# Kernel tuning notes

Hardware: AMD Instinct MI355X
Metric: run time of the kernel (lower is better)

The kernel has to match this reference:

```python
import jax, jax.numpy as jnp
import numpy as np

B, S, D, H = 4, 8192, 1024, 16
DH = D // H  # attention head size


def setup_inputs() -> dict:
    key = jax.random.key(0)
    ks = jax.random.split(key, 12)
    sc = 0.02
    return {
        "hidden_states": jax.random.normal(ks[0], (B, S, D), jnp.float32),
        "attention_mask": jnp.zeros((B, 1, S), jnp.float32),
        "Wq": jax.random.normal(ks[1], (D, D), jnp.float32) * sc,
        "bq": jnp.zeros((D,), jnp.float32),
        "Wqa": jax.random.normal(ks[2], (D, H), jnp.float32) * sc,
        "bqa": jnp.zeros((H,), jnp.float32),
        "Wk": jax.random.normal(ks[3], (D, D), jnp.float32) * sc,
        "bk": jnp.zeros((D,), jnp.float32),
        "Wka": jax.random.normal(ks[4], (D, H), jnp.float32) * sc,
        "bka": jnp.zeros((H,), jnp.float32),
        "Wt": jax.random.normal(ks[5], (D, D), jnp.float32) * sc,
        "bt": jnp.zeros((D,), jnp.float32),
    }


def reference(hidden_states, attention_mask, Wq, bq, Wqa, bqa, Wk, bk, Wka, bka, Wt, bt):
    b, s, _ = hidden_states.shape
    scale = 1.0 / np.sqrt(DH).astype(np.float32)

    mixed_q = hidden_states @ Wq + bq            # [B,S,D]
    mixed_k = hidden_states @ Wk + bk            # [B,S,D]

    # query attention pooling: scores [B,H,S]
    q_score = (mixed_q @ Wqa + bqa).transpose(0, 2, 1) * scale + attention_mask
    q_weight = jax.nn.softmax(q_score, axis=-1)  # [B,H,S]

    q_heads = mixed_q.reshape(b, s, H, DH)       # [B,S,H,DH]
    pooled_q = jnp.einsum("bhs,bshd->bhd", q_weight, q_heads)  # [B,H,DH]
    pooled_q = pooled_q.reshape(b, 1, D)         # global query vector per batch

    mixed_qk = mixed_k * pooled_q                # [B,S,D]

    qk_score = (mixed_qk @ Wka + bka).transpose(0, 2, 1) * scale + attention_mask
    qk_weight = jax.nn.softmax(qk_score, axis=-1)  # [B,H,S]

    k_heads = mixed_qk.reshape(b, s, H, DH)
    pooled_k = jnp.einsum("bhs,bshd->bhd", qk_weight, k_heads)  # [B,H,DH]

    weighted = (q_heads * pooled_k[:, None, :, :]).reshape(b, s, D)  # [B,S,D]
    return weighted @ Wt + bt + mixed_q
```

## Files before the change

### kernel.cpp

```cpp
#include <hip/hip_runtime.h>
#include <hip/hip_bf16.h>
#include <stdint.h>

typedef __hip_bfloat16 bf16;
typedef __attribute__((ext_vector_type(8))) short bf16x8v;
typedef __attribute__((ext_vector_type(4))) float f32x4v;

#define B_   4
#define S_   8192
#define D_   1024
#define H_   16
#define DH_  64
#define M_TOT (B_ * S_)

__device__ __forceinline__ float bf2f(bf16 x) { return __bfloat162float(x); }
__device__ __forceinline__ bf16  f2bf(float x) { return __float2bfloat16(x); }

__device__ __forceinline__ void storev(float* p, float v) { *p = v; }
__device__ __forceinline__ void storev(bf16* p, float v) { *p = f2bf(v); }

__device__ __forceinline__ void async_copy16(const void* g, void* l) {
  __builtin_amdgcn_global_load_lds(
      (const __attribute__((address_space(1))) unsigned int*)g,
      (__attribute__((address_space(3))) unsigned int*)l,
      16, 0, 0);
}

#define VMCNT(n) asm volatile("s_waitcnt vmcnt(" #n ")" ::: "memory")
__device__ __forceinline__ void barrier_() {
  asm volatile("" ::: "memory");
  __builtin_amdgcn_s_barrier();
  asm volatile("" ::: "memory");
}

__global__ __launch_bounds__(256) void f2bf_kernel(
    const float* __restrict__ in, bf16* __restrict__ out, int n4)
{
  const int i = blockIdx.x * 256 + threadIdx.x;
  if (i >= n4) return;
  const float4 v = ((const float4*)in)[i];
  union { bf16 h[4]; uint64_t u; } pk;
  pk.h[0] = f2bf(v.x); pk.h[1] = f2bf(v.y);
  pk.h[2] = f2bf(v.z); pk.h[3] = f2bf(v.w);
  ((uint64_t*)out)[i] = pk.u;
}

#define STAGE_A(nb, h, k0) do { \
  async_copy16(gA + (size_t)((h) * 64      ) * sA + (size_t)(k0) * 2, smem + (nb) + (h) * 16384 + ldsw); \
  async_copy16(gA + (size_t)((h) * 64 + 128) * sA + (size_t)(k0) * 2, smem + (nb) + (h) * 16384 + 8192 + ldsw); \
} while (0)

#define STAGE_B(nb, h, k0) do { \
  async_copy16(gB + (size_t)((h) * 32      ) * sB + (size_t)(k0) * 2, smem + (nb) + 32768 + (h) * 16384 + ldsw); \
  async_copy16(gB + (size_t)((h) * 32 + 128) * sB + (size_t)(k0) * 2, smem + (nb) + 32768 + (h) * 16384 + 8192 + ldsw); \
} while (0)

#define READ_A(mh) do { \
  _Pragma("unroll") for (int il = 0; il < 4; ++il) { \
    const uint8_t* p_ = Ab + (mh) * 16384 + (wr * 64 + il * 16 + l16) * 128; \
    a[il][0] = *(const bf16x8v*)(p_ + k0off); \
    a[il][1] = *(const bf16x8v*)(p_ + k1off); } \
} while (0)

#define READ_B(nh, BR) do { \
  _Pragma("unroll") for (int jl = 0; jl < 2; ++jl) { \
    const uint8_t* p_ = Bb + 32768 + (nh) * 16384 + (wc * 32 + jl * 16 + l16) * 128; \
    BR[jl][0] = *(const bf16x8v*)(p_ + k0off); \
    BR[jl][1] = *(const bf16x8v*)(p_ + k1off); } \
} while (0)

#define MFMA_Q(IOFF, JOFF, BR) do { \
  _Pragma("unroll") for (int il = 0; il < 4; ++il) \
  _Pragma("unroll") for (int jl = 0; jl < 2; ++jl) \
  _Pragma("unroll") for (int kk = 0; kk < 2; ++kk) \
    acc[(IOFF) + il][(JOFF) + jl] = __builtin_amdgcn_mfma_f32_16x16x32_bf16( \
        a[il][kk], BR[jl][kk], acc[(IOFF) + il][(JOFF) + jl], 0, 0, 0); \
} while (0)

template <typename OutT>
__global__ __launch_bounds__(512, 2) void gemm256_kernel(
    const bf16* __restrict__ A, int lda, const bf16* __restrict__ BT,
    const float* __restrict__ bias0, const float* __restrict__ bias1,
    const bf16* addC, int ldadd,
    OutT* __restrict__ C, int ldc, int M, int Ncols, int K, int perBatchB)
{
  extern __shared__ __align__(16) uint8_t smem[];

  const int ntile = Ncols >> 8;
  const int mtiles = M >> 8;
  const int xcd = blockIdx.x & 7;
  const int local = blockIdx.x >> 3;
  const int tn = local % ntile;
  const int tm = xcd * (mtiles >> 3) + local / ntile;
  const int m0 = tm << 8, n0 = tn << 8;
  const bf16* Bt = BT + (perBatchB ? (size_t)(m0 >> 13) * (size_t)Ncols * (size_t)K : 0);

  const int tid = threadIdx.x, w = tid >> 6, lane = tid & 63;
  const int quad = lane >> 4, l16 = lane & 15;
  const int wr = w >> 2, wc = w & 3;
  const int lr = lane >> 3, ls = lane & 7;

  const size_t sA = (size_t)lda * 2, sB = (size_t)K * 2;
  const int srcslot = (ls ^ lr) << 4;
  const uint8_t* gA = (const uint8_t*)A  + (size_t)(m0 + 8 * w + lr) * sA + srcslot;
  const uint8_t* gB = (const uint8_t*)Bt + (size_t)(n0 + 64 * wr + 8 * wc + lr) * sB + srcslot;
  const int ldsw = w << 10;

  const int e7 = l16 & 7;
  const int k0off = (quad ^ e7) << 4;
  const int k1off = ((quad + 4) ^ e7) << 4;

  f32x4v acc[8][4] = {};
  bf16x8v a[4][2], b0[2][2], b1[2][2];

  const int NT = K >> 6;

  STAGE_A(0, 0, 0);
  STAGE_B(0, 0, 0);
  STAGE_B(0, 1, 0);
  STAGE_A(0, 1, 0);
  VMCNT(4);
  barrier_();

  for (int t = 0; t < NT; ++t) {
    const int buf = (t & 1) << 16;
    const int nbuf = buf ^ 65536;
    const int kst = (t + 1 < NT ? t + 1 : t) << 6;
    const uint8_t* Ab = smem + buf;
    const uint8_t* Bb = smem + buf;

    READ_A(0);
    READ_B(0, b0);
    STAGE_A(nbuf, 0, kst);
    barrier_();
    __builtin_amdgcn_s_setprio(1);
    MFMA_Q(0, 0, b0);
    __builtin_amdgcn_s_setprio(0);
    VMCNT(4);
    barrier_();

    READ_B(1, b1);
    STAGE_B(nbuf, 0, kst);
    barrier_();
    __builtin_amdgcn_s_setprio(1);
    MFMA_Q(0, 2, b1);
    __builtin_amdgcn_s_setprio(0);
    VMCNT(4);
    barrier_();

    READ_A(1);
    STAGE_B(nbuf, 1, kst);
    barrier_();
    __builtin_amdgcn_s_setprio(1);
    MFMA_Q(4, 2, b1);
    __builtin_amdgcn_s_setprio(0);
    barrier_();

    STAGE_A(nbuf, 1, kst);
    barrier_();
    __builtin_amdgcn_s_setprio(1);
    MFMA_Q(4, 0, b0);
    __builtin_amdgcn_s_setprio(0);
    VMCNT(4);
    barrier_();
  }
  VMCNT(0);

#pragma unroll
  for (int ai = 0; ai < 8; ++ai) {
    const int row = m0 + wr * 128 + ai * 16 + quad * 4;
#pragma unroll
    for (int jb = 0; jb < 4; ++jb) {
      const int col = n0 + wc * 64 + jb * 16 + l16;
      const float bb = (col < 1024) ? (bias0 ? bias0[col] : 0.f)
                                    : (bias1 ? bias1[col - 1024] : 0.f);
      f32x4v v = acc[ai][jb];
#pragma unroll
      for (int r = 0; r < 4; ++r) {
        float o = v[r] + bb;
        if (addC) o += bf2f(addC[(size_t)(row + r) * ldadd + col]);
        storev(&C[(size_t)(row + r) * ldc + col], o);
      }
    }
  }
}

__global__ __launch_bounds__(256) void score_kernel(
    const bf16* __restrict__ X, int ldx, const bf16* __restrict__ WaT,
    float* __restrict__ scores, int perBatchW)
{
  const int tid = threadIdx.x, wave = tid >> 6, lane = tid & 63;
  const int quad = lane >> 4, l16 = lane & 15;
  const int row0 = blockIdx.x * 64 + wave * 16;
  const int b = row0 / S_;
  const bf16* W = WaT + (perBatchW ? (size_t)b * H_ * D_ : 0);
  const bf16* arow = X + (size_t)(row0 + l16) * ldx;
  const bf16* brow = W + (size_t)l16 * D_;
  f32x4v acc = {};
  for (int k0 = 0; k0 < D_; k0 += 32) {
    bf16x8v av = *(const bf16x8v*)(arow + k0 + quad * 8);
    bf16x8v bv = *(const bf16x8v*)(brow + k0 + quad * 8);
    acc = __builtin_amdgcn_mfma_f32_16x16x32_bf16(av, bv, acc, 0, 0, 0);
  }
  const int srel = (row0 % S_) + quad * 4;
  float* orow = scores + ((size_t)b * H_ + l16) * S_ + srel;
#pragma unroll
  for (int r = 0; r < 4; r++) orow[r] = acc[r];
}

__global__ __launch_bounds__(256) void stats_kernel(
    const float* __restrict__ sc, const float* __restrict__ mask,
    float scale, float* __restrict__ stats)
{
  const int bh = blockIdx.x, b = bh >> 4, tid = threadIdx.x;
  const float* row = sc + (size_t)bh * S_;
  const float* mrow = mask + (size_t)b * S_;
  __shared__ float red[256];
  float m = -3.4e38f;
  for (int s = tid; s < S_; s += 256) m = fmaxf(m, row[s] * scale + mrow[s]);
  red[tid] = m; __syncthreads();
  for (int o = 128; o > 0; o >>= 1) { if (tid < o) red[tid] = fmaxf(red[tid], red[tid + o]); __syncthreads(); }
  const float M = red[0]; __syncthreads();
  float sum = 0.f;
  for (int s = tid; s < S_; s += 256) sum += expf(row[s] * scale + mrow[s] - M);
  red[tid] = sum; __syncthreads();
  for (int o = 128; o > 0; o >>= 1) { if (tid < o) red[tid] += red[tid + o]; __syncthreads(); }
  if (tid == 0) { stats[bh * 2] = M; stats[bh * 2 + 1] = red[0]; }
}

__global__ __launch_bounds__(256) void pool_kernel(
    const float* __restrict__ sc, const float* __restrict__ mask,
    const float* __restrict__ stats, const bf16* __restrict__ X, int ldx,
    float* __restrict__ pooled, float scale)
{
  const int bh = blockIdx.x, chunk = blockIdx.y;
  const int b = bh >> 4, h = bh & 15;
  const int dh = threadIdx.x & 63, sr = threadIdx.x >> 6;
  const float M = stats[bh * 2], inv = 1.f / stats[bh * 2 + 1];
  const float* row = sc + (size_t)bh * S_;
  const float* mrow = mask + (size_t)b * S_;
  float acc = 0.f;
  const int s0 = chunk * 256;
  for (int s = s0 + sr; s < s0 + 256; s += 4) {
    float w = expf(row[s] * scale + mrow[s] - M) * inv;
    acc += w * bf2f(X[((size_t)b * S_ + s) * ldx + h * DH_ + dh]);
  }
  __shared__ float red[256];
  red[threadIdx.x] = acc; __syncthreads();
  if (sr == 0)
    atomicAdd(&pooled[b * D_ + h * DH_ + dh],
              red[dh] + red[64 + dh] + red[128 + dh] + red[192 + dh]);
}

__global__ __launch_bounds__(256) void prep_wa_kernel(
    const float* __restrict__ Wa, const float* __restrict__ pq,
    bf16* __restrict__ out, int nb)
{
  const int idx = blockIdx.x * 256 + threadIdx.x;
  if (idx >= nb * H_ * D_) return;
  const int d = idx & (D_ - 1);
  const int h = (idx >> 10) & 15;
  const int b = idx >> 14;
  float v = Wa[d * H_ + h];
  if (pq) v *= pq[b * D_ + d];
  out[idx] = f2bf(v);
}

__global__ __launch_bounds__(1024) void transpose_kernel(
    const float* __restrict__ W, bf16* __restrict__ WT)
{
  __shared__ float t[32][33];
  const int tx = threadIdx.x, ty = threadIdx.y;
  const int bx = blockIdx.x, by = blockIdx.y;
  t[ty][tx] = W[(size_t)(by * 32 + ty) * D_ + bx * 32 + tx];
  __syncthreads();
  WT[(size_t)(bx * 32 + ty) * D_ + by * 32 + tx] = f2bf(t[tx][ty]);
}

__global__ __launch_bounds__(1024) void transpose_scale_kernel(
    const float* __restrict__ W, const float* __restrict__ pq,
    const float* __restrict__ pk, bf16* __restrict__ out)
{
  __shared__ float t[32][33];
  const int tx = threadIdx.x, ty = threadIdx.y;
  const int bx = blockIdx.x, by = blockIdx.y, b = blockIdx.z;
  t[ty][tx] = W[(size_t)(by * 32 + ty) * D_ + bx * 32 + tx];
  __syncthreads();
  const int n = bx * 32 + ty, k = by * 32 + tx;
  const float s = pq[b * D_ + k] * pk[b * D_ + k];
  out[(size_t)b * D_ * D_ + (size_t)n * D_ + k] = f2bf(t[tx][ty] * s);
}

namespace {
struct LdsAttrInit {
  LdsAttrInit() {
    (void)hipFuncSetAttribute(reinterpret_cast<const void*>(&gemm256_kernel<bf16>),
                              hipFuncAttributeMaxDynamicSharedMemorySize, 131072);
    (void)hipFuncSetAttribute(reinterpret_cast<const void*>(&gemm256_kernel<float>),
                              hipFuncAttributeMaxDynamicSharedMemorySize, 131072);
  }
};
LdsAttrInit ldsAttrInit_;
}

extern "C" void kernel_launch(void* const* d_in, const int* in_sizes, int n_in,
                              void* d_out, int out_size, void* d_ws, size_t ws_size,
                              hipStream_t stream)
{
  const float* hs   = (const float*)d_in[0];
  const float* mask = (const float*)d_in[1];
  const float* Wq   = (const float*)d_in[2];
  const float* bq   = (const float*)d_in[3];
  const float* Wqa  = (const float*)d_in[4];
  const float* Wk   = (const float*)d_in[6];
  const float* bk   = (const float*)d_in[7];
  const float* Wka  = (const float*)d_in[8];
  const float* Wt   = (const float*)d_in[10];
  const float* bt   = (const float*)d_in[11];
  float* out = (float*)d_out;

  uint8_t* w = (uint8_t*)d_ws;
  bf16*  hs_bf     = (bf16*)(w + 0);
  bf16*  mixed_qk  = (bf16*)(w + 67108864);
  bf16*  WqkT      = (bf16*)(w + 201326592);
  bf16*  WtTs      = (bf16*)(w + 205520896);
  bf16*  WaqT      = (bf16*)(w + 213909504);
  bf16*  WakTs     = (bf16*)(w + 213942272);
  float* scores_q  = (float*)(w + 214073344);
  float* scores_qk = (float*)(w + 216170496);
  float* stats_q   = (float*)(w + 218267648);
  float* stats_qk  = (float*)(w + 218268160);
  float* pq_raw    = (float*)(w + 218268672);
  float* pk_raw    = (float*)(w + 218285056);

  const bf16* mixed_q = mixed_qk;
  const bf16* mixed_k = mixed_qk + 1024;
  const int LDQK = 2048;

  const float scale = 0.125f;
  dim3 tblk(32, 32);

  f2bf_kernel<<<(M_TOT * D_ / 4 + 255) / 256, 256, 0, stream>>>(hs, hs_bf, M_TOT * D_ / 4);

  transpose_kernel<<<dim3(32, 32), tblk, 0, stream>>>(Wq, WqkT);
  transpose_kernel<<<dim3(32, 32), tblk, 0, stream>>>(Wk, WqkT + 1024 * 1024);

  gemm256_kernel<bf16><<<1024, 512, 131072, stream>>>(
      hs_bf, 1024, WqkT, bq, bk, nullptr, 0, mixed_qk, LDQK, M_TOT, 2048, D_, 0);

  hipMemsetAsync(pq_raw, 0, 2 * D_ * B_ * sizeof(float), stream);

  prep_wa_kernel<<<64, 256, 0, stream>>>(Wqa, nullptr, WaqT, 1);
  score_kernel<<<512, 256, 0, stream>>>(mixed_q, LDQK, WaqT, scores_q, 0);
  stats_kernel<<<64, 256, 0, stream>>>(scores_q, mask, scale, stats_q);
  pool_kernel<<<dim3(64, 32), 256, 0, stream>>>(scores_q, mask, stats_q, mixed_q, LDQK, pq_raw, scale);

  prep_wa_kernel<<<256, 256, 0, stream>>>(Wka, pq_raw, WakTs, 4);
  score_kernel<<<512, 256, 0, stream>>>(mixed_k, LDQK, WakTs, scores_qk, 1);
  stats_kernel<<<64, 256, 0, stream>>>(scores_qk, mask, scale, stats_qk);
  pool_kernel<<<dim3(64, 32), 256, 0, stream>>>(scores_qk, mask, stats_qk, mixed_k, LDQK, pk_raw, scale);

  transpose_scale_kernel<<<dim3(32, 32, 4), tblk, 0, stream>>>(Wt, pq_raw, pk_raw, WtTs);

  gemm256_kernel<float><<<512, 512, 131072, stream>>>(
      mixed_q, LDQK, WtTs, bt, nullptr, mixed_q, LDQK, out, D_, M_TOT, D_, D_, 1);
}
```

Baseline: 626.3 us.

## Drop softmax max pass, defer normalization, and merge prep kernels into one launch

The score kernel now writes exp(score*scale+mask) directly. The pool kernel accumulates the weighted sums and the per-head weight totals with atomics, and normalization moves into the downstream weight-scaling kernels, so the separate stats kernels go away. The f32-to-bf16 cast, the two weight transposes and the Wqa prep are folded into a single launch to save launches and a pass over the scores. Skipping the max subtraction risks overflow for large scores or extreme mask values.

```diff
diff --git a/kernel.cpp b/kernel.cpp
--- a/kernel.cpp
+++ b/kernel.cpp
@@ -33,16 +33,41 @@
   asm volatile("" ::: "memory");
 }
 
-__global__ __launch_bounds__(256) void f2bf_kernel(
-    const float* __restrict__ in, bf16* __restrict__ out, int n4)
-{
-  const int i = blockIdx.x * 256 + threadIdx.x;
-  if (i >= n4) return;
-  const float4 v = ((const float4*)in)[i];
-  union { bf16 h[4]; uint64_t u; } pk;
-  pk.h[0] = f2bf(v.x); pk.h[1] = f2bf(v.y);
-  pk.h[2] = f2bf(v.z); pk.h[3] = f2bf(v.w);
-  ((uint64_t*)out)[i] = pk.u;
+__global__ __launch_bounds__(256) void prep_kernel(
+    const float* __restrict__ hs, const float* __restrict__ Wq,
+    const float* __restrict__ Wk, const float* __restrict__ Wqa,
+    bf16* __restrict__ hs_bf, bf16* __restrict__ WqkT, bf16* __restrict__ WaqT)
+{
+  __shared__ float tset[32][33];
+  const int blk = blockIdx.x, tid = threadIdx.x;
+  if (blk < 2048) {
+    const int n4 = M_TOT * D_ / 4;
+    for (int i = blk * 256 + tid; i < n4; i += 2048 * 256) {
+      const float4 v = ((const float4*)hs)[i];
+      union { bf16 h[4]; uint64_t u; } pk;
+      pk.h[0] = f2bf(v.x); pk.h[1] = f2bf(v.y);
+      pk.h[2] = f2bf(v.z); pk.h[3] = f2bf(v.w);
+      ((uint64_t*)hs_bf)[i] = pk.u;
+    }
+  } else if (blk < 4096) {
+    const int t = blk - 2048;
+    const int mat = t >> 10, tile = t & 1023;
+    const int bx = tile & 31, by = tile >> 5;
+    const float* W = mat ? Wk : Wq;
+    bf16* o = WqkT + (size_t)mat * 1024 * 1024;
+    const int tx = tid & 31, ty0 = tid >> 5;
+#pragma unroll
+    for (int r = 0; r < 4; ++r)
+      tset[ty0 + 8 * r][tx] = W[(size_t)(by * 32 + ty0 + 8 * r) * D_ + bx * 32 + tx];
+    __syncthreads();
+#pragma unroll
+    for (int r = 0; r < 4; ++r)
+      o[(size_t)(bx * 32 + ty0 + 8 * r) * D_ + by * 32 + tx] = f2bf(tset[tx][ty0 + 8 * r]);
+  } else {
+    const int idx = (blk - 4096) * 256 + tid;
+    const int d = idx & (D_ - 1), h = (idx >> 10) & 15;
+    WaqT[idx] = f2bf(Wqa[d * H_ + h]);
+  }
 }
 
 #define STAGE_A(nb, h, k0) do { \
@@ -187,7 +212,8 @@
 
 __global__ __launch_bounds__(256) void score_kernel(
     const bf16* __restrict__ X, int ldx, const bf16* __restrict__ WaT,
-    float* __restrict__ scores, int perBatchW)
+    const float* __restrict__ mask, float* __restrict__ scores,
+    float scale, int perBatchW)
 {
   const int tid = threadIdx.x, wave = tid >> 6, lane = tid & 63;
   const int quad = lane >> 4, l16 = lane & 15;
@@ -203,83 +229,57 @@
     acc = __builtin_amdgcn_mfma_f32_16x16x32_bf16(av, bv, acc, 0, 0, 0);
   }
   const int srel = (row0 % S_) + quad * 4;
+  const float* mp = mask + (size_t)b * S_ + srel;
   float* orow = scores + ((size_t)b * H_ + l16) * S_ + srel;
 #pragma unroll
-  for (int r = 0; r < 4; r++) orow[r] = acc[r];
-}
-
-__global__ __launch_bounds__(256) void stats_kernel(
-    const float* __restrict__ sc, const float* __restrict__ mask,
-    float scale, float* __restrict__ stats)
-{
-  const int bh = blockIdx.x, b = bh >> 4, tid = threadIdx.x;
-  const float* row = sc + (size_t)bh * S_;
-  const float* mrow = mask + (size_t)b * S_;
-  __shared__ float red[256];
-  float m = -3.4e38f;
-  for (int s = tid; s < S_; s += 256) m = fmaxf(m, row[s] * scale + mrow[s]);
-  red[tid] = m; __syncthreads();
-  for (int o = 128; o > 0; o >>= 1) { if (tid < o) red[tid] = fmaxf(red[tid], red[tid + o]); __syncthreads(); }
-  const float M = red[0]; __syncthreads();
-  float sum = 0.f;
-  for (int s = tid; s < S_; s += 256) sum += expf(row[s] * scale + mrow[s] - M);
-  red[tid] = sum; __syncthreads();
-  for (int o = 128; o > 0; o >>= 1) { if (tid < o) red[tid] += red[tid + o]; __syncthreads(); }
-  if (tid == 0) { stats[bh * 2] = M; stats[bh * 2 + 1] = red[0]; }
+  for (int r = 0; r < 4; r++) orow[r] = expf(acc[r] * scale + mp[r]);
 }
 
 __global__ __launch_bounds__(256) void pool_kernel(
-    const float* __restrict__ sc, const float* __restrict__ mask,
-    const float* __restrict__ stats, const bf16* __restrict__ X, int ldx,
-    float* __restrict__ pooled, float scale)
+    const float* __restrict__ esc, const bf16* __restrict__ X, int ldx,
+    float* __restrict__ pooled, float* __restrict__ sumw)
 {
   const int bh = blockIdx.x, chunk = blockIdx.y;
   const int b = bh >> 4, h = bh & 15;
   const int dh = threadIdx.x & 63, sr = threadIdx.x >> 6;
-  const float M = stats[bh * 2], inv = 1.f / stats[bh * 2 + 1];
-  const float* row = sc + (size_t)bh * S_;
-  const float* mrow = mask + (size_t)b * S_;
-  float acc = 0.f;
+  const float* erow = esc + (size_t)bh * S_;
+  float acc = 0.f, accw = 0.f;
   const int s0 = chunk * 256;
   for (int s = s0 + sr; s < s0 + 256; s += 4) {
-    float w = expf(row[s] * scale + mrow[s] - M) * inv;
-    acc += w * bf2f(X[((size_t)b * S_ + s) * ldx + h * DH_ + dh]);
+    const float e = erow[s];
+    acc += e * bf2f(X[((size_t)b * S_ + s) * ldx + h * DH_ + dh]);
+    if (dh == 0) accw += e;
   }
   __shared__ float red[256];
-  red[threadIdx.x] = acc; __syncthreads();
+  __shared__ float rw[4];
+  red[threadIdx.x] = acc;
+  if (dh == 0) rw[sr] = accw;
+  __syncthreads();
   if (sr == 0)
     atomicAdd(&pooled[b * D_ + h * DH_ + dh],
               red[dh] + red[64 + dh] + red[128 + dh] + red[192 + dh]);
+  if (threadIdx.x == 0)
+    atomicAdd(&sumw[bh], rw[0] + rw[1] + rw[2] + rw[3]);
 }
 
 __global__ __launch_bounds__(256) void prep_wa_kernel(
     const float* __restrict__ Wa, const float* __restrict__ pq,
-    bf16* __restrict__ out, int nb)
+    const float* __restrict__ sw, bf16* __restrict__ out)
 {
   const int idx = blockIdx.x * 256 + threadIdx.x;
-  if (idx >= nb * H_ * D_) return;
+  if (idx >= B_ * H_ * D_) return;
   const int d = idx & (D_ - 1);
   const int h = (idx >> 10) & 15;
   const int b = idx >> 14;
-  float v = Wa[d * H_ + h];
-  if (pq) v *= pq[b * D_ + d];
+  const float inv = __frcp_rn(sw[b * H_ + (d >> 6)]);
+  const float v = Wa[d * H_ + h] * pq[b * D_ + d] * inv;
   out[idx] = f2bf(v);
-}
-
-__global__ __launch_bounds__(1024) void transpose_kernel(
-    const float* __restrict__ W, bf16* __restrict__ WT)
-{
-  __shared__ float t[32][33];
-  const int tx = threadIdx.x, ty = threadIdx.y;
-  const int bx = blockIdx.x, by = blockIdx.y;
-  t[ty][tx] = W[(size_t)(by * 32 + ty) * D_ + bx * 32 + tx];
-  __syncthreads();
-  WT[(size_t)(bx * 32 + ty) * D_ + by * 32 + tx] = f2bf(t[tx][ty]);
 }
 
 __global__ __launch_bounds__(1024) void transpose_scale_kernel(
     const float* __restrict__ W, const float* __restrict__ pq,
-    const float* __restrict__ pk, bf16* __restrict__ out)
+    const float* __restrict__ swq, const float* __restrict__ pk,
+    const float* __restrict__ swk, bf16* __restrict__ out)
 {
   __shared__ float t[32][33];
   const int tx = threadIdx.x, ty = threadIdx.y;
@@ -287,7 +287,9 @@
   t[ty][tx] = W[(size_t)(by * 32 + ty) * D_ + bx * 32 + tx];
   __syncthreads();
   const int n = bx * 32 + ty, k = by * 32 + tx;
-  const float s = pq[b * D_ + k] * pk[b * D_ + k];
+  const float invq = __frcp_rn(swq[b * H_ + (k >> 6)]);
+  const float invk = __frcp_rn(swk[b * H_ + (k >> 6)]);
+  const float s = (pq[b * D_ + k] * invq) * (pk[b * D_ + k] * invk);
   out[(size_t)b * D_ * D_ + (size_t)n * D_ + k] = f2bf(t[tx][ty] * s);
 }
 
@@ -328,10 +330,10 @@
   bf16*  WakTs     = (bf16*)(w + 213942272);
   float* scores_q  = (float*)(w + 214073344);
   float* scores_qk = (float*)(w + 216170496);
-  float* stats_q   = (float*)(w + 218267648);
-  float* stats_qk  = (float*)(w + 218268160);
-  float* pq_raw    = (float*)(w + 218268672);
-  float* pk_raw    = (float*)(w + 218285056);
+  float* pq_raw    = (float*)(w + 218267648);
+  float* pk_raw    = (float*)(w + 218284032);
+  float* sumw_q    = (float*)(w + 218300416);
+  float* sumw_k    = (float*)(w + 218300672);
 
   const bf16* mixed_q = mixed_qk;
   const bf16* mixed_k = mixed_qk + 1024;
@@ -340,27 +342,22 @@
   const float scale = 0.125f;
   dim3 tblk(32, 32);
 
-  f2bf_kernel<<<(M_TOT * D_ / 4 + 255) / 256, 256, 0, stream>>>(hs, hs_bf, M_TOT * D_ / 4);
-
-  transpose_kernel<<<dim3(32, 32), tblk, 0, stream>>>(Wq, WqkT);
-  transpose_kernel<<<dim3(32, 32), tblk, 0, stream>>>(Wk, WqkT + 1024 * 1024);
+  hipMemsetAsync(pq_raw, 0, 2 * 16384 + 512, stream);
+
+  prep_kernel<<<4160, 256, 0, stream>>>(hs, Wq, Wk, Wqa, hs_bf, WqkT, WaqT);
 
   gemm256_kernel<bf16><<<1024, 512, 131072, stream>>>(
       hs_bf, 1024, WqkT, bq, bk, nullptr, 0, mixed_qk, LDQK, M_TOT, 2048, D_, 0);
 
-  hipMemsetAsync(pq_raw, 0, 2 * D_ * B_ * sizeof(float), stream);
-
-  prep_wa_kernel<<<64, 256, 0, stream>>>(Wqa, nullptr, WaqT, 1);
-  score_kernel<<<512, 256, 0, stream>>>(mixed_q, LDQK, WaqT, scores_q, 0);
-  stats_kernel<<<64, 256, 0, stream>>>(scores_q, mask, scale, stats_q);
-  pool_kernel<<<dim3(64, 32), 256, 0, stream>>>(scores_q, mask, stats_q, mixed_q, LDQK, pq_raw, scale);
-
-  prep_wa_kernel<<<256, 256, 0, stream>>>(Wka, pq_raw, WakTs, 4);
-  score_kernel<<<512, 256, 0, stream>>>(mixed_k, LDQK, WakTs, scores_qk, 1);
-  stats_kernel<<<64, 256, 0, stream>>>(scores_qk, mask, scale, stats_qk);
-  pool_kernel<<<dim3(64, 32), 256, 0, stream>>>(scores_qk, mask, stats_qk, mixed_k, LDQK, pk_raw, scale);
-
-  transpose_scale_kernel<<<dim3(32, 32, 4), tblk, 0, stream>>>(Wt, pq_raw, pk_raw, WtTs);
+  score_kernel<<<512, 256, 0, stream>>>(mixed_q, LDQK, WaqT, mask, scores_q, scale, 0);
+  pool_kernel<<<dim3(64, 32), 256, 0, stream>>>(scores_q, mixed_q, LDQK, pq_raw, sumw_q);
+
+  prep_wa_kernel<<<256, 256, 0, stream>>>(Wka, pq_raw, sumw_q, WakTs);
+  score_kernel<<<512, 256, 0, stream>>>(mixed_k, LDQK, WakTs, mask, scores_qk, scale, 1);
+  pool_kernel<<<dim3(64, 32), 256, 0, stream>>>(scores_qk, mixed_k, LDQK, pk_raw, sumw_k);
+
+  transpose_scale_kernel<<<dim3(32, 32, 4), tblk, 0, stream>>>(
+      Wt, pq_raw, sumw_q, pk_raw, sumw_k, WtTs);
 
   gemm256_kernel<float><<<512, 512, 131072, stream>>>(
       mixed_q, LDQK, WtTs, bt, nullptr, mixed_q, LDQK, out, D_, M_TOT, D_, D_, 1);
```

New measurement: 608.5 us. 1.03x faster.
